# Kernel tuning notes

Measured on AMD Instinct MI355X. Metric: run time of the kernel, lower is better.

Reference implementation:

```python
import jax, jax.numpy as jnp
import numpy as np

B, C, L = 32, 64, 512
PATCH_LEN = 16
PATCH_NUM = L // PATCH_LEN
H = 512          # hidden_dim
FF = 512         # moe_d_ff == hidden_dim per __init__
E = 8            # num_experts
TOP_K = 2


def setup_inputs() -> dict:
    key = jax.random.key(0)
    ks = jax.random.split(key, 8)
    s = 0.02
    return {
        "x": jax.random.normal(ks[0], (B, C, L), dtype=jnp.float32),
        "Wp": jax.random.normal(ks[1], (H, PATCH_LEN), dtype=jnp.float32) * s,
        "bp": jnp.zeros((H,), dtype=jnp.float32),
        "Wg": jax.random.normal(ks[2], (E, H), dtype=jnp.float32) * s,
        "Wgate": jax.random.normal(ks[3], (E, FF, H), dtype=jnp.float32) * s,
        "Wup": jax.random.normal(ks[4], (E, FF, H), dtype=jnp.float32) * s,
        "Wdown": jax.random.normal(ks[5], (E, H, FF), dtype=jnp.float32) * s,
    }


def reference(x, Wp, bp, Wg, Wgate, Wup, Wdown):
    b, c, l = x.shape
    # patchify: [B, C, P, patch_len] -> project to hidden
    p = x.reshape(b, c, PATCH_NUM, PATCH_LEN)
    h = jnp.einsum("bcpl,dl->bcpd", p, Wp) + bp          # [B,C,P,H]
    tokens = h.reshape(-1, H)                               # [T,H]
    T = tokens.shape[0]

    # router: softmax in fp32, then top-k (norm_topk_prob=False)
    logits = tokens @ Wg.T                                   # [T,E]
    rw = jax.nn.softmax(logits.astype(jnp.float32), axis=-1)
    topw, topi = jax.lax.top_k(rw, TOP_K)                    # [T,K]

    # dense per-(token,expert) combine weight, equiv. to gather/scatter combine
    w = jnp.zeros((T, E), dtype=jnp.float32)
    w = w.at[jnp.arange(T)[:, None], topi].add(topw)         # [T,E]

    out = jnp.zeros((T, H), dtype=tokens.dtype)
    for e in range(E):  # fixed small expert loop
        g = jax.nn.silu(tokens @ Wgate[e].T)
        u = tokens @ Wup[e].T
        y = (g * u) @ Wdown[e].T                             # [T,H]
        out = out + (w[:, e:e + 1] * y.astype(jnp.float32)).astype(tokens.dtype)

    return out.reshape(b, c * PATCH_NUM, H)
```

## Files before the change

### kernel.cpp

```cpp
#include <hip/hip_runtime.h>
#include <hip/hip_bf16.h>
#include <cstdint>
#include <cstddef>

typedef __attribute__((ext_vector_type(8))) short short8;
typedef __attribute__((ext_vector_type(4))) float f32x4;

#define GLL16(g, l) __builtin_amdgcn_global_load_lds(                         \
    (const __attribute__((address_space(1))) void*)(g),                        \
    (__attribute__((address_space(3))) void*)(l), 16, 0, 0)

constexpr int kB = 32, kC = 64, kL = 512;
constexpr int kPL = 16, kPN = 32;
constexpr int kH = 512, kFF = 512, kE = 8;
constexpr int kT = kB * kC * kPN;
constexpr int kTilesPerSlot = 520;
constexpr int kMaxTiles = 2 * kTilesPerSlot;
constexpr int kMaxPairs = kMaxTiles * 128;

constexpr size_t OFF_TOK  = 0;
constexpr size_t OFF_GU   = OFF_TOK + (size_t)kT * kH * 2;
constexpr size_t OFF_TOPI = OFF_GU + (size_t)kMaxPairs * kFF * 2;
constexpr size_t OFF_TOPW = OFF_TOPI + (size_t)kT * 4;
constexpr size_t OFF_CCNT = OFF_TOPW + (size_t)kT * 8;
constexpr size_t OFF_COFF = OFF_CCNT + 256 * 16 * 4;
constexpr size_t OFF_EOFF = OFF_COFF + 256 * 16 * 4;
constexpr size_t OFF_TILE = OFF_EOFF + 256;
constexpr size_t OFF_PTOK = OFF_TILE + ((kMaxTiles * 4 + 255) & ~255ull);
constexpr size_t OFF_PW   = OFF_PTOK + (size_t)kMaxPairs * 4;
constexpr size_t OFF_DUMP = OFF_PW + (size_t)kMaxPairs * 4;
constexpr size_t OFF_BG   = OFF_DUMP + 128 * 512 * 4;
constexpr size_t OFF_BU   = OFF_BG + (size_t)kE * kFF * kH * 2;
constexpr size_t OFF_BD   = OFF_BU + (size_t)kE * kFF * kH * 2;
constexpr size_t OFF_WC   = OFF_BD + (size_t)kE * kH * kFF * 2;
constexpr size_t OFF_BC   = OFF_WC + 8 * 16 * 8;

__global__ __launch_bounds__(256) void k_conv3(const float* __restrict__ a,
                                               const float* __restrict__ b,
                                               const float* __restrict__ c,
                                               __hip_bfloat16* __restrict__ da,
                                               __hip_bfloat16* __restrict__ db,
                                               __hip_bfloat16* __restrict__ dc, int n) {
  for (int i = blockIdx.x * blockDim.x + threadIdx.x; i < 3 * n; i += gridDim.x * blockDim.x) {
    int reg = i / n, j = i - reg * n;
    const float* s = (reg == 0) ? a : (reg == 1) ? b : c;
    __hip_bfloat16* d = (reg == 0) ? da : (reg == 1) ? db : dc;
    d[j] = __float2bfloat16(s[j]);
  }
}

__global__ void k_wcomb(const float* __restrict__ Wg, const float* __restrict__ Wp,
                        const float* __restrict__ bp, double* __restrict__ wc,
                        double* __restrict__ bc) {
  int tid = threadIdx.x;
  int e = tid >> 4, l = tid & 15;
  double s = 0.0;
  for (int d = 0; d < kH; ++d) s += (double)Wg[e * kH + d] * (double)Wp[d * kPL + l];
  wc[e * kPL + l] = s;
  if (l == 0) {
    double b = 0.0;
    for (int d = 0; d < kH; ++d) b += (double)Wg[e * kH + d] * (double)bp[d];
    bc[e] = b;
  }
}

__global__ __launch_bounds__(256) void k_patch(const float* __restrict__ x,
                                               const float* __restrict__ Wp,
                                               const float* __restrict__ bp,
                                               __hip_bfloat16* __restrict__ tok) {
  __shared__ float sWp[512 * 17];
  __shared__ float sx[128];
  __shared__ float sbp[512];
  int bb = blockIdx.x;
  int bc = bb >> 2, pg = bb & 3;
  int tid = threadIdx.x;
  for (int i = tid; i < 512 * 16; i += 256) sWp[(i >> 4) * 17 + (i & 15)] = Wp[i];
  if (tid < 128) sx[tid] = x[(size_t)bc * 512 + pg * 128 + tid];
  for (int i = tid; i < 512; i += 256) sbp[i] = bp[i];
  __syncthreads();
  for (int tl = 0; tl < 8; ++tl) {
    int t = bc * kPN + pg * 8 + tl;
    const float* xp = &sx[tl * 16];
    for (int d = tid; d < 512; d += 256) {
      float s = sbp[d];
#pragma unroll
      for (int l = 0; l < 16; ++l) s += xp[l] * sWp[d * 17 + l];
      tok[(size_t)t * kH + d] = __float2bfloat16(s);
    }
  }
}

__global__ __launch_bounds__(256) void k_router(const float* __restrict__ x,
                                                const double* __restrict__ wc,
                                                const double* __restrict__ bc,
                                                int* __restrict__ topi,
                                                float* __restrict__ topw,
                                                int* __restrict__ chunkCnt) {
  int t = blockIdx.x * 256 + threadIdx.x;
  int bci = t >> 5, p = t & 31;
  const float* xp = &x[(size_t)bci * 512 + p * 16];
  double xl[16];
#pragma unroll
  for (int l = 0; l < 16; ++l) xl[l] = (double)xp[l];
  double lo[8];
  double m = -1e300;
#pragma unroll
  for (int e = 0; e < 8; ++e) {
    double s = bc[e];
#pragma unroll
    for (int l = 0; l < 16; ++l) s += xl[l] * wc[e * 16 + l];
    lo[e] = s;
    m = fmax(m, s);
  }
  double den = 0.0;
#pragma unroll
  for (int e = 0; e < 8; ++e) {
    lo[e] = exp(lo[e] - m);
    den += lo[e];
  }
  int i1 = 0;
  double v1 = lo[0];
#pragma unroll
  for (int e = 1; e < 8; ++e)
    if (lo[e] > v1) { v1 = lo[e]; i1 = e; }
  int i2 = -1;
  double v2 = -1.0;
#pragma unroll
  for (int e = 0; e < 8; ++e)
    if (e != i1 && lo[e] > v2) { v2 = lo[e]; i2 = e; }
  topi[t] = i1 | (i2 << 4);
  topw[2 * t] = (float)(v1 / den);
  topw[2 * t + 1] = (float)(v2 / den);

  __shared__ int wsum[16][4];
  int wave = threadIdx.x >> 6, lane = threadIdx.x & 63;
#pragma unroll
  for (int seg = 0; seg < 16; ++seg) {
    int e = seg & 7;
    bool sel = (seg < 8) ? (i1 == e) : (i2 == e);
    unsigned long long mm = __ballot(sel);
    if (lane == 0) wsum[seg][wave] = __popcll(mm);
  }
  __syncthreads();
  if (threadIdx.x < 16)
    chunkCnt[blockIdx.x * 16 + threadIdx.x] =
        wsum[threadIdx.x][0] + wsum[threadIdx.x][1] + wsum[threadIdx.x][2] + wsum[threadIdx.x][3];
}

__global__ __launch_bounds__(256) void k_scan(const int* __restrict__ chunkCnt,
                                              int* __restrict__ chunkOff,
                                              int* __restrict__ eoff,
                                              int* __restrict__ tileExpert,
                                              int* __restrict__ pairTok,
                                              float* __restrict__ pairW) {
  int tid = threadIdx.x;
  __shared__ int cnt[256 * 16];
  __shared__ int coff[256 * 16];
  for (int i = tid; i < 256 * 16; i += 256) cnt[i] = chunkCnt[i];
  __syncthreads();
  __shared__ int totals[16];
  __shared__ int base[16];
  __shared__ int padded[16];
  if (tid < 16) {
    int run = 0;
    for (int c = 0; c < 256; ++c) {
      coff[c * 16 + tid] = run;
      run += cnt[c * 16 + tid];
    }
    totals[tid] = run;
  }
  __syncthreads();
  for (int i = tid; i < 256 * 16; i += 256) chunkOff[i] = coff[i];
  if (tid == 0) {
    for (int s = 0; s < 2; ++s) {
      int b = s * kTilesPerSlot * 128;
      for (int e = 0; e < 8; ++e) {
        int seg = s * 8 + e;
        base[seg] = b;
        padded[seg] = (totals[seg] + 127) & ~127;
        b += padded[seg];
      }
    }
  }
  __syncthreads();
  if (tid < 16) eoff[tid] = base[tid];
  for (int tI = tid; tI < kMaxTiles; tI += 256) tileExpert[tI] = -1;
  __syncthreads();
  for (int seg = 0; seg < 16; ++seg) {
    int e = seg & 7;
    int tile0 = base[seg] >> 7, nt = padded[seg] >> 7;
    for (int tI = tid; tI < nt; tI += 256) tileExpert[tile0 + tI] = e;
    for (int p = base[seg] + totals[seg] + tid; p < base[seg] + padded[seg]; p += 256) {
      pairTok[p] = -1;
      pairW[p] = 0.f;
    }
  }
}

__global__ __launch_bounds__(256) void k_fill(const int* __restrict__ topi,
                                              const float* __restrict__ topw,
                                              const int* __restrict__ chunkOff,
                                              const int* __restrict__ eoff,
                                              int* __restrict__ pairTok,
                                              float* __restrict__ pairW) {
  int chunk = blockIdx.x;
  int t = chunk * 256 + threadIdx.x;
  int pk = topi[t];
  int i1 = pk & 15, i2 = (pk >> 4) & 15;
  float w1 = topw[2 * t], w2 = topw[2 * t + 1];
  int wave = threadIdx.x >> 6, lane = threadIdx.x & 63;
  __shared__ int wsum[16][4];
  int pre[16];
  bool sel[16];
#pragma unroll
  for (int seg = 0; seg < 16; ++seg) {
    int e = seg & 7;
    sel[seg] = (seg < 8) ? (i1 == e) : (i2 == e);
    unsigned long long mm = __ballot(sel[seg]);
    pre[seg] = __popcll(mm & ((1ull << lane) - 1));
    if (lane == 0) wsum[seg][wave] = __popcll(mm);
  }
  __syncthreads();
#pragma unroll
  for (int seg = 0; seg < 16; ++seg) {
    if (!sel[seg]) continue;
    int woff = 0;
    for (int w = 0; w < wave; ++w) woff += wsum[seg][w];
    int pos = eoff[seg] + chunkOff[chunk * 16 + seg] + woff + pre[seg];
    pairTok[pos] = t;
    pairW[pos] = (seg < 8) ? w1 : w2;
  }
}


__global__ __launch_bounds__(256, 2) void k_gateup_sp(const __hip_bfloat16* __restrict__ tok,
                                                      const __hip_bfloat16* __restrict__ Wg0,
                                                      const __hip_bfloat16* __restrict__ Wu0,
                                                      const int* __restrict__ pairTok,
                                                      const int* __restrict__ tileExpert,
                                                      __hip_bfloat16* __restrict__ GU) {
  const int tileIdx = blockIdx.x >> 2;
  const int e = tileExpert[tileIdx];
  if (e < 0) return;
  __shared__ __hip_bfloat16 As[2][128 * 32];
  __shared__ __hip_bfloat16 Bgs[2][128 * 32];
  __shared__ __hip_bfloat16 Bus[2][128 * 32];
  const int tid = threadIdx.x;
  const int wid = tid >> 6, lane = tid & 63;
  const int tileBase = tileIdx * 128, tileN = (blockIdx.x & 3) * 128;
  const int wr = wid >> 1, wcol = wid & 1;
  const int r = lane & 15, kq = lane >> 4;

  f32x4 accg[4][4] = {};
  f32x4 accu[4][4] = {};

  const char* Ab = (const char*)tok;
  const char* Bgb = (const char*)(Wg0 + (size_t)e * kFF * kH);
  const char* Bub = (const char*)(Wu0 + (size_t)e * kFF * kH);
  const int off0 = wid * 1024 + lane * 16;
  const int row0 = off0 >> 6;
  const int col0 = ((((off0 >> 4) & 3) ^ ((row0 >> 1) & 3)) << 4);
  const int off1 = off0 + 4096;
  const int row1 = off1 >> 6;
  const int col1 = ((((off1 >> 4) & 3) ^ ((row1 >> 1) & 3)) << 4);
  int t0i = pairTok[tileBase + row0];
  int t1i = pairTok[tileBase + row1];
  const size_t t0 = (size_t)(t0i < 0 ? 0 : t0i);
  const size_t t1 = (size_t)(t1i < 0 ? 0 : t1i);

  auto STAGE = [&](int buf, int kt) {
    const int kb = kt * 64;
    char* as = (char*)As[buf];
    char* bgs = (char*)Bgs[buf];
    char* bus = (char*)Bus[buf];
    GLL16(Ab + t0 * 1024 + kb + col0, as + wid * 1024);
    GLL16(Ab + t1 * 1024 + kb + col1, as + 4096 + wid * 1024);
    GLL16(Bgb + (size_t)(tileN + row0) * 1024 + kb + col0, bgs + wid * 1024);
    GLL16(Bgb + (size_t)(tileN + row1) * 1024 + kb + col1, bgs + 4096 + wid * 1024);
    GLL16(Bub + (size_t)(tileN + row0) * 1024 + kb + col0, bus + wid * 1024);
    GLL16(Bub + (size_t)(tileN + row1) * 1024 + kb + col1, bus + 4096 + wid * 1024);
  };

  STAGE(0, 0);

#pragma unroll 1
  for (int kt = 0; kt < 16; ++kt) {
    const int cur = kt & 1;
    if (kt < 15) {
      STAGE(cur ^ 1, kt + 1);
      asm volatile("s_waitcnt vmcnt(6)" ::: "memory");
    } else {
      asm volatile("s_waitcnt vmcnt(0)" ::: "memory");
    }
    __builtin_amdgcn_s_barrier();
    __builtin_amdgcn_sched_barrier(0);

    short8 a[4], bg[4], bu[4];
#pragma unroll
    for (int i = 0; i < 4; ++i) {
      int row = wr * 64 + i * 16 + r;
      int sc = (kq ^ ((row >> 1) & 3)) << 3;
      a[i] = *(const short8*)&As[cur][row * 32 + sc];
    }
#pragma unroll
    for (int j = 0; j < 4; ++j) {
      int row = wcol * 64 + j * 16 + r;
      int sc = (kq ^ ((row >> 1) & 3)) << 3;
      bg[j] = *(const short8*)&Bgs[cur][row * 32 + sc];
      bu[j] = *(const short8*)&Bus[cur][row * 32 + sc];
    }
#pragma unroll
    for (int i = 0; i < 4; ++i)
#pragma unroll
      for (int j = 0; j < 4; ++j) {
        accg[i][j] = __builtin_amdgcn_mfma_f32_16x16x32_bf16(a[i], bg[j], accg[i][j], 0, 0, 0);
        accu[i][j] = __builtin_amdgcn_mfma_f32_16x16x32_bf16(a[i], bu[j], accu[i][j], 0, 0, 0);
      }
    __builtin_amdgcn_s_barrier();
  }

#pragma unroll
  for (int i = 0; i < 4; ++i)
#pragma unroll
    for (int j = 0; j < 4; ++j)
#pragma unroll
      for (int q = 0; q < 4; ++q) {
        int row = tileBase + wr * 64 + i * 16 + kq * 4 + q;
        int col = tileN + wcol * 64 + j * 16 + r;
        float g = accg[i][j][q], u = accu[i][j][q];
        float val = g / (1.f + __expf(-g)) * u;
        GU[(size_t)row * kFF + col] = __float2bfloat16(val);
      }
}

__global__ __launch_bounds__(256, 2) void k_down_sp(const __hip_bfloat16* __restrict__ GU,
                                                    const __hip_bfloat16* __restrict__ Wd0,
                                                    const int* __restrict__ pairTok,
                                                    const float* __restrict__ pairW,
                                                    const int* __restrict__ tileExpert,
                                                    float* __restrict__ out,
                                                    float* __restrict__ dump,
                                                    int tileOff, int first) {
  const int tile = tileOff + (blockIdx.x >> 2);
  const int e = tileExpert[tile];
  if (e < 0) return;
  __shared__ __hip_bfloat16 As[2][128 * 32];
  __shared__ __hip_bfloat16 Bs[2][128 * 32];
  __shared__ float Cs[32 * 132];
  const int tid = threadIdx.x;
  const int wid = tid >> 6, lane = tid & 63;
  const int tileBase = tile * 128, tileN = (blockIdx.x & 3) * 128;
  const int wr = wid >> 1, wcol = wid & 1;
  const int r = lane & 15, kq = lane >> 4;

  f32x4 acc[4][4] = {};

  const char* Ab = (const char*)GU;
  const char* Bb = (const char*)(Wd0 + (size_t)e * kH * kFF);
  const int off0 = wid * 1024 + lane * 16;
  const int row0 = off0 >> 6;
  const int col0 = ((((off0 >> 4) & 3) ^ ((row0 >> 1) & 3)) << 4);
  const int off1 = off0 + 4096;
  const int row1 = off1 >> 6;
  const int col1 = ((((off1 >> 4) & 3) ^ ((row1 >> 1) & 3)) << 4);

  auto STAGE = [&](int buf, int kt) {
    const int kb = kt * 64;
    char* as = (char*)As[buf];
    char* bs = (char*)Bs[buf];
    GLL16(Ab + (size_t)(tileBase + row0) * 1024 + kb + col0, as + wid * 1024);
    GLL16(Ab + (size_t)(tileBase + row1) * 1024 + kb + col1, as + 4096 + wid * 1024);
    GLL16(Bb + (size_t)(tileN + row0) * 1024 + kb + col0, bs + wid * 1024);
    GLL16(Bb + (size_t)(tileN + row1) * 1024 + kb + col1, bs + 4096 + wid * 1024);
  };

  STAGE(0, 0);

#pragma unroll 1
  for (int kt = 0; kt < 16; ++kt) {
    const int cur = kt & 1;
    if (kt < 15) {
      STAGE(cur ^ 1, kt + 1);
      asm volatile("s_waitcnt vmcnt(4)" ::: "memory");
    } else {
      asm volatile("s_waitcnt vmcnt(0)" ::: "memory");
    }
    __builtin_amdgcn_s_barrier();
    __builtin_amdgcn_sched_barrier(0);

    short8 a[4], b[4];
#pragma unroll
    for (int i = 0; i < 4; ++i) {
      int row = wr * 64 + i * 16 + r;
      int sc = (kq ^ ((row >> 1) & 3)) << 3;
      a[i] = *(const short8*)&As[cur][row * 32 + sc];
    }
#pragma unroll
    for (int j = 0; j < 4; ++j) {
      int row = wcol * 64 + j * 16 + r;
      int sc = (kq ^ ((row >> 1) & 3)) << 3;
      b[j] = *(const short8*)&Bs[cur][row * 32 + sc];
    }
#pragma unroll
    for (int i = 0; i < 4; ++i)
#pragma unroll
      for (int j = 0; j < 4; ++j)
        acc[i][j] = __builtin_amdgcn_mfma_f32_16x16x32_bf16(a[i], b[j], acc[i][j], 0, 0, 0);
    __builtin_amdgcn_s_barrier();
  }

  const int rowl = tid >> 3;
  const int cbase = (tid & 7) * 16;
#pragma unroll
  for (int batch = 0; batch < 4; ++batch) {
    __syncthreads();
    if (wr == (batch >> 1)) {
      int bi0 = (batch & 1) * 2;
#pragma unroll
      for (int ii = 0; ii < 2; ++ii) {
        int i = bi0 + ii;
#pragma unroll
        for (int j = 0; j < 4; ++j) {
          int cl = wcol * 64 + j * 16 + r;
#pragma unroll
          for (int q = 0; q < 4; ++q) {
            int rl = ii * 16 + kq * 4 + q;
            Cs[rl * 132 + cl] = acc[i][j][q];
          }
        }
      }
    }
    __syncthreads();
    int prow = tileBase + batch * 32 + rowl;
    float wv = pairW[prow];
    int tk = pairTok[prow];
    float* orow = (tk >= 0) ? out + (size_t)tk * kH + tileN + cbase
                            : dump + (size_t)(prow & 127) * kH + tileN + cbase;
    const float* crow = &Cs[rowl * 132 + cbase];
#pragma unroll
    for (int c = 0; c < 4; ++c) {
      f32x4 v = *(const f32x4*)(crow + c * 4);
      v *= wv;
      if (first) {
        *(f32x4*)(orow + c * 4) = v;
      } else {
        f32x4 o = *(const f32x4*)(orow + c * 4);
        *(f32x4*)(orow + c * 4) = o + v;
      }
    }
  }
}

extern "C" void kernel_launch(void* const* d_in, const int* in_sizes, int n_in,
                              void* d_out, int out_size, void* d_ws, size_t ws_size,
                              hipStream_t stream) {
  const float* x = (const float*)d_in[0];
  const float* Wp = (const float*)d_in[1];
  const float* bp = (const float*)d_in[2];
  const float* Wg = (const float*)d_in[3];
  const float* Wgate = (const float*)d_in[4];
  const float* Wup = (const float*)d_in[5];
  const float* Wdown = (const float*)d_in[6];
  float* out = (float*)d_out;

  char* ws = (char*)d_ws;
  __hip_bfloat16* tok = (__hip_bfloat16*)(ws + OFF_TOK);
  __hip_bfloat16* gu = (__hip_bfloat16*)(ws + OFF_GU);
  int* topi = (int*)(ws + OFF_TOPI);
  float* topw = (float*)(ws + OFF_TOPW);
  int* chunkCnt = (int*)(ws + OFF_CCNT);
  int* chunkOff = (int*)(ws + OFF_COFF);
  int* eoff = (int*)(ws + OFF_EOFF);
  int* tileExpert = (int*)(ws + OFF_TILE);
  int* pairTok = (int*)(ws + OFF_PTOK);
  float* pairW = (float*)(ws + OFF_PW);
  float* dump = (float*)(ws + OFF_DUMP);
  __hip_bfloat16* bgw = (__hip_bfloat16*)(ws + OFF_BG);
  __hip_bfloat16* buw = (__hip_bfloat16*)(ws + OFF_BU);
  __hip_bfloat16* bdw = (__hip_bfloat16*)(ws + OFF_BD);
  double* wc = (double*)(ws + OFF_WC);
  double* bcv = (double*)(ws + OFF_BC);

  const int nw = kE * kFF * kH;
  k_conv3<<<3072, 256, 0, stream>>>(Wgate, Wup, Wdown, bgw, buw, bdw, nw);
  k_wcomb<<<1, 128, 0, stream>>>(Wg, Wp, bp, wc, bcv);
  k_patch<<<8192, 256, 0, stream>>>(x, Wp, bp, tok);
  k_router<<<256, 256, 0, stream>>>(x, wc, bcv, topi, topw, chunkCnt);
  k_scan<<<1, 256, 0, stream>>>(chunkCnt, chunkOff, eoff, tileExpert, pairTok, pairW);
  k_fill<<<256, 256, 0, stream>>>(topi, topw, chunkOff, eoff, pairTok, pairW);

  k_gateup_sp<<<kMaxTiles * 4, 256, 0, stream>>>(tok, bgw, buw, pairTok, tileExpert, gu);
  k_down_sp<<<kTilesPerSlot * 4, 256, 0, stream>>>(gu, bdw, pairTok, pairW, tileExpert, out,
                                                   dump, 0, 1);
  k_down_sp<<<kTilesPerSlot * 4, 256, 0, stream>>>(gu, bdw, pairTok, pairW, tileExpert, out,
                                                   dump, kTilesPerSlot, 0);
}
```

Measured before the change: 529.0 us.

## Replace double-buffered BK=32 pipeline with single-buffered BK=64 tiles in expert GEMMs

Both the gate/up and the down-projection kernels drop the two-stage double-buffered LDS pipeline (K step 32) for a single buffer holding a K step of 64, with a new 8-way XOR swizzle. Each iteration issues all global-to-LDS loads, synchronizes, then runs two MFMA sub-steps, which halves the number of barriers per tile. The trade-off is that the next tile's loads no longer overlap with compute, so global latency is exposed, though it is hidden only if two resident blocks per CU interleave well.

```diff
diff --git a/kernel.cpp b/kernel.cpp
--- a/kernel.cpp
+++ b/kernel.cpp
@@ -242,9 +242,9 @@
   const int tileIdx = blockIdx.x >> 2;
   const int e = tileExpert[tileIdx];
   if (e < 0) return;
-  __shared__ __hip_bfloat16 As[2][128 * 32];
-  __shared__ __hip_bfloat16 Bgs[2][128 * 32];
-  __shared__ __hip_bfloat16 Bus[2][128 * 32];
+  __shared__ __hip_bfloat16 As[128 * 64];
+  __shared__ __hip_bfloat16 Bgs[128 * 64];
+  __shared__ __hip_bfloat16 Bus[128 * 64];
   const int tid = threadIdx.x;
   const int wid = tid >> 6, lane = tid & 63;
   const int tileBase = tileIdx * 128, tileN = (blockIdx.x & 3) * 128;
@@ -257,66 +257,57 @@
   const char* Ab = (const char*)tok;
   const char* Bgb = (const char*)(Wg0 + (size_t)e * kFF * kH);
   const char* Bub = (const char*)(Wu0 + (size_t)e * kFF * kH);
-  const int off0 = wid * 1024 + lane * 16;
-  const int row0 = off0 >> 6;
-  const int col0 = ((((off0 >> 4) & 3) ^ ((row0 >> 1) & 3)) << 4);
-  const int off1 = off0 + 4096;
-  const int row1 = off1 >> 6;
-  const int col1 = ((((off1 >> 4) & 3) ^ ((row1 >> 1) & 3)) << 4);
-  int t0i = pairTok[tileBase + row0];
-  int t1i = pairTok[tileBase + row1];
-  const size_t t0 = (size_t)(t0i < 0 ? 0 : t0i);
-  const size_t t1 = (size_t)(t1i < 0 ? 0 : t1i);
-
-  auto STAGE = [&](int buf, int kt) {
-    const int kb = kt * 64;
-    char* as = (char*)As[buf];
-    char* bgs = (char*)Bgs[buf];
-    char* bus = (char*)Bus[buf];
-    GLL16(Ab + t0 * 1024 + kb + col0, as + wid * 1024);
-    GLL16(Ab + t1 * 1024 + kb + col1, as + 4096 + wid * 1024);
-    GLL16(Bgb + (size_t)(tileN + row0) * 1024 + kb + col0, bgs + wid * 1024);
-    GLL16(Bgb + (size_t)(tileN + row1) * 1024 + kb + col1, bgs + 4096 + wid * 1024);
-    GLL16(Bub + (size_t)(tileN + row0) * 1024 + kb + col0, bus + wid * 1024);
-    GLL16(Bub + (size_t)(tileN + row1) * 1024 + kb + col1, bus + 4096 + wid * 1024);
-  };
-
-  STAGE(0, 0);
+
+  int rowS[4], colS[4];
+  size_t tokS[4];
+#pragma unroll
+  for (int s = 0; s < 4; ++s) {
+    int off = wid * 1024 + lane * 16 + s * 4096;
+    rowS[s] = off >> 7;
+    int p = (off & 127) >> 4;
+    colS[s] = ((p ^ (rowS[s] & 7)) << 4);
+    int ti = pairTok[tileBase + rowS[s]];
+    tokS[s] = (size_t)(ti < 0 ? 0 : ti);
+  }
 
 #pragma unroll 1
-  for (int kt = 0; kt < 16; ++kt) {
-    const int cur = kt & 1;
-    if (kt < 15) {
-      STAGE(cur ^ 1, kt + 1);
-      asm volatile("s_waitcnt vmcnt(6)" ::: "memory");
-    } else {
-      asm volatile("s_waitcnt vmcnt(0)" ::: "memory");
-    }
-    __builtin_amdgcn_s_barrier();
-    __builtin_amdgcn_sched_barrier(0);
-
-    short8 a[4], bg[4], bu[4];
-#pragma unroll
-    for (int i = 0; i < 4; ++i) {
-      int row = wr * 64 + i * 16 + r;
-      int sc = (kq ^ ((row >> 1) & 3)) << 3;
-      a[i] = *(const short8*)&As[cur][row * 32 + sc];
-    }
-#pragma unroll
-    for (int j = 0; j < 4; ++j) {
-      int row = wcol * 64 + j * 16 + r;
-      int sc = (kq ^ ((row >> 1) & 3)) << 3;
-      bg[j] = *(const short8*)&Bgs[cur][row * 32 + sc];
-      bu[j] = *(const short8*)&Bus[cur][row * 32 + sc];
-    }
-#pragma unroll
-    for (int i = 0; i < 4; ++i)
+  for (int kt = 0; kt < 8; ++kt) {
+    const int kb = kt * 128;
+#pragma unroll
+    for (int s = 0; s < 4; ++s) {
+      GLL16(Ab + tokS[s] * 1024 + kb + colS[s], (char*)As + wid * 1024 + s * 4096);
+      GLL16(Bgb + (size_t)(tileN + rowS[s]) * 1024 + kb + colS[s],
+            (char*)Bgs + wid * 1024 + s * 4096);
+      GLL16(Bub + (size_t)(tileN + rowS[s]) * 1024 + kb + colS[s],
+            (char*)Bus + wid * 1024 + s * 4096);
+    }
+    __syncthreads();
+
+#pragma unroll
+    for (int kk = 0; kk < 2; ++kk) {
+      short8 a[4], bg[4], bu[4];
+#pragma unroll
+      for (int i = 0; i < 4; ++i) {
+        int row = wr * 64 + i * 16 + r;
+        int pc = (kk * 4 + kq) ^ (row & 7);
+        a[i] = *(const short8*)&As[row * 64 + pc * 8];
+      }
 #pragma unroll
       for (int j = 0; j < 4; ++j) {
-        accg[i][j] = __builtin_amdgcn_mfma_f32_16x16x32_bf16(a[i], bg[j], accg[i][j], 0, 0, 0);
-        accu[i][j] = __builtin_amdgcn_mfma_f32_16x16x32_bf16(a[i], bu[j], accu[i][j], 0, 0, 0);
-      }
-    __builtin_amdgcn_s_barrier();
+        int row = wcol * 64 + j * 16 + r;
+        int pc = (kk * 4 + kq) ^ (row & 7);
+        bg[j] = *(const short8*)&Bgs[row * 64 + pc * 8];
+        bu[j] = *(const short8*)&Bus[row * 64 + pc * 8];
+      }
+#pragma unroll
+      for (int i = 0; i < 4; ++i)
+#pragma unroll
+        for (int j = 0; j < 4; ++j) {
+          accg[i][j] = __builtin_amdgcn_mfma_f32_16x16x32_bf16(a[i], bg[j], accg[i][j], 0, 0, 0);
+          accu[i][j] = __builtin_amdgcn_mfma_f32_16x16x32_bf16(a[i], bu[j], accu[i][j], 0, 0, 0);
+        }
+    }
+    __syncthreads();
   }
 
 #pragma unroll
@@ -344,8 +335,8 @@
   const int tile = tileOff + (blockIdx.x >> 2);
   const int e = tileExpert[tile];
   if (e < 0) return;
-  __shared__ __hip_bfloat16 As[2][128 * 32];
-  __shared__ __hip_bfloat16 Bs[2][128 * 32];
+  __shared__ __hip_bfloat16 As[128 * 64];
+  __shared__ __hip_bfloat16 Bs[128 * 64];
   __shared__ float Cs[32 * 132];
   const int tid = threadIdx.x;
   const int wid = tid >> 6, lane = tid & 63;
@@ -357,56 +348,50 @@
 
   const char* Ab = (const char*)GU;
   const char* Bb = (const char*)(Wd0 + (size_t)e * kH * kFF);
-  const int off0 = wid * 1024 + lane * 16;
-  const int row0 = off0 >> 6;
-  const int col0 = ((((off0 >> 4) & 3) ^ ((row0 >> 1) & 3)) << 4);
-  const int off1 = off0 + 4096;
-  const int row1 = off1 >> 6;
-  const int col1 = ((((off1 >> 4) & 3) ^ ((row1 >> 1) & 3)) << 4);
-
-  auto STAGE = [&](int buf, int kt) {
-    const int kb = kt * 64;
-    char* as = (char*)As[buf];
-    char* bs = (char*)Bs[buf];
-    GLL16(Ab + (size_t)(tileBase + row0) * 1024 + kb + col0, as + wid * 1024);
-    GLL16(Ab + (size_t)(tileBase + row1) * 1024 + kb + col1, as + 4096 + wid * 1024);
-    GLL16(Bb + (size_t)(tileN + row0) * 1024 + kb + col0, bs + wid * 1024);
-    GLL16(Bb + (size_t)(tileN + row1) * 1024 + kb + col1, bs + 4096 + wid * 1024);
-  };
-
-  STAGE(0, 0);
+
+  int rowS[4], colS[4];
+#pragma unroll
+  for (int s = 0; s < 4; ++s) {
+    int off = wid * 1024 + lane * 16 + s * 4096;
+    rowS[s] = off >> 7;
+    int p = (off & 127) >> 4;
+    colS[s] = ((p ^ (rowS[s] & 7)) << 4);
+  }
 
 #pragma unroll 1
-  for (int kt = 0; kt < 16; ++kt) {
-    const int cur = kt & 1;
-    if (kt < 15) {
-      STAGE(cur ^ 1, kt + 1);
-      asm volatile("s_waitcnt vmcnt(4)" ::: "memory");
-    } else {
-      asm volatile("s_waitcnt vmcnt(0)" ::: "memory");
-    }
-    __builtin_amdgcn_s_barrier();
-    __builtin_amdgcn_sched_barrier(0);
-
-    short8 a[4], b[4];
-#pragma unroll
-    for (int i = 0; i < 4; ++i) {
-      int row = wr * 64 + i * 16 + r;
-      int sc = (kq ^ ((row >> 1) & 3)) << 3;
-      a[i] = *(const short8*)&As[cur][row * 32 + sc];
-    }
-#pragma unroll
-    for (int j = 0; j < 4; ++j) {
-      int row = wcol * 64 + j * 16 + r;
-      int sc = (kq ^ ((row >> 1) & 3)) << 3;
-      b[j] = *(const short8*)&Bs[cur][row * 32 + sc];
-    }
-#pragma unroll
-    for (int i = 0; i < 4; ++i)
-#pragma unroll
-      for (int j = 0; j < 4; ++j)
-        acc[i][j] = __builtin_amdgcn_mfma_f32_16x16x32_bf16(a[i], b[j], acc[i][j], 0, 0, 0);
-    __builtin_amdgcn_s_barrier();
+  for (int kt = 0; kt < 8; ++kt) {
+    const int kb = kt * 128;
+#pragma unroll
+    for (int s = 0; s < 4; ++s) {
+      GLL16(Ab + (size_t)(tileBase + rowS[s]) * 1024 + kb + colS[s],
+            (char*)As + wid * 1024 + s * 4096);
+      GLL16(Bb + (size_t)(tileN + rowS[s]) * 1024 + kb + colS[s],
+            (char*)Bs + wid * 1024 + s * 4096);
+    }
+    __syncthreads();
+
+#pragma unroll
+    for (int kk = 0; kk < 2; ++kk) {
+      short8 a[4], b[4];
+#pragma unroll
+      for (int i = 0; i < 4; ++i) {
+        int row = wr * 64 + i * 16 + r;
+        int pc = (kk * 4 + kq) ^ (row & 7);
+        a[i] = *(const short8*)&As[row * 64 + pc * 8];
+      }
+#pragma unroll
+      for (int j = 0; j < 4; ++j) {
+        int row = wcol * 64 + j * 16 + r;
+        int pc = (kk * 4 + kq) ^ (row & 7);
+        b[j] = *(const short8*)&Bs[row * 64 + pc * 8];
+      }
+#pragma unroll
+      for (int i = 0; i < 4; ++i)
+#pragma unroll
+        for (int j = 0; j < 4; ++j)
+          acc[i][j] = __builtin_amdgcn_mfma_f32_16x16x32_bf16(a[i], b[j], acc[i][j], 0, 0, 0);
+    }
+    __syncthreads();
   }
 
   const int rowl = tid >> 3;
```

Result: faster. 492.5 us (-6.9%).
